# Kernel tuning notes

Hardware: AMD Instinct MI355X
Metric: run time of the kernel (lower is better)

The kernel has to match this reference:

```python
import jax, jax.numpy as jnp
import numpy as np

DIM = 1024
HEADS = 16
HEAD_DIM = DIM // HEADS


def setup_inputs() -> dict:
    key = jax.random.key(0)
    ks = jax.random.split(key, 9)
    s = 1.0 / np.sqrt(DIM)
    return {
        "x": jax.random.normal(ks[0], (2, 2048, DIM), dtype=jnp.float32),
        "Wq": jax.random.normal(ks[1], (DIM, DIM), dtype=jnp.float32) * s,
        "bq": jnp.zeros((DIM,), dtype=jnp.float32),
        "Wk": jax.random.normal(ks[2], (DIM, DIM), dtype=jnp.float32) * s,
        "bk": jnp.zeros((DIM,), dtype=jnp.float32),
        "Wv": jax.random.normal(ks[3], (DIM, DIM), dtype=jnp.float32) * s,
        "bv": jnp.zeros((DIM,), dtype=jnp.float32),
        "Wo": jax.random.normal(ks[4], (DIM, DIM), dtype=jnp.float32) * s,
        "bo": jnp.zeros((DIM,), dtype=jnp.float32),
    }


def reference(x, Wq, bq, Wk, bk, Wv, bv, Wo, bo):
    B, S, D = x.shape
    H, Dh = HEADS, HEAD_DIM

    def split_heads(t):  # (B,S,D) -> (B,H,S,Dh)
        return t.reshape(B, S, H, Dh).transpose(0, 2, 1, 3)

    q = split_heads(x @ Wq + bq)
    k = split_heads(x @ Wk + bk)
    v = split_heads(x @ Wv + bv)

    scores = jnp.einsum("bhsd,bhtd->bhst", q, k) / np.sqrt(Dh).astype(x.dtype)
    attn = jax.nn.softmax(scores, axis=-1)
    ctx = jnp.einsum("bhst,bhtd->bhsd", attn, v)
    ctx = ctx.transpose(0, 2, 1, 3).reshape(B, S, D)
    return ctx @ Wo + bo
```

## Files before the change

### kernel.cpp

```cpp
#include <hip/hip_runtime.h>
#include <hip/hip_bf16.h>
#include <cstdint>

typedef __bf16 bf16;
typedef __bf16 bf16x8 __attribute__((ext_vector_type(8)));
typedef float f32x4 __attribute__((ext_vector_type(4)));
typedef float f32x8 __attribute__((ext_vector_type(8)));
typedef float f32x16 __attribute__((ext_vector_type(16)));

#define DIM   1024
#define SEQ   2048
#define BATCH 2
#define HEADS 16
#define HDIM  64

#define QSCALE 0.1803368801111204f

__device__ __forceinline__ void gload_lds16(const void* g, void* l) {
    __builtin_amdgcn_global_load_lds(
        (const __attribute__((address_space(1))) void*)g,
        (__attribute__((address_space(3))) void*)l,
        16, 0, 0);
}

__device__ __forceinline__ uint32_t pkbf(float a, float b) {
    union { bf16 h[2]; uint32_t u; } t;
    t.h[0] = (bf16)a; t.h[1] = (bf16)b;
    return t.u;
}

#define LO8(v)  __builtin_shufflevector(v, v, 0, 1, 2, 3, 4, 5, 6, 7)
#define HI8(v)  __builtin_shufflevector(v, v, 8, 9, 10, 11, 12, 13, 14, 15)
#define LO4(v)  __builtin_shufflevector(v, v, 0, 1, 2, 3)
#define HI4(v)  __builtin_shufflevector(v, v, 4, 5, 6, 7)

__global__ __launch_bounds__(256) void cvt_wt_kernel(const float* __restrict__ Wq,
                                                     const float* __restrict__ Wk,
                                                     const float* __restrict__ Wv,
                                                     const float* __restrict__ Wo,
                                                     bf16* __restrict__ Wt) {
    int z = blockIdx.z;
    const float* W = (z == 0) ? Wq : (z == 1) ? Wk : (z == 2) ? Wv : Wo;
    bf16* out = Wt + (size_t)z * DIM * DIM;
    int w = threadIdx.x >> 6, lane = threadIdx.x & 63;
    int n  = blockIdx.x * 64 + lane;
    int kb = blockIdx.y * 32 + w * 8;
    bf16x8 o;
#pragma unroll
    for (int j = 0; j < 8; ++j)
        o[j] = (bf16)W[(size_t)(kb + j) * DIM + n];
    *(bf16x8*)(out + (size_t)n * DIM + kb) = o;
}

template <int MODE>
__global__ __launch_bounds__(256) void gemm128_kernel(
        const void* __restrict__ Ap,
        const bf16* __restrict__ WtB,
        const float* __restrict__ b0,
        const float* __restrict__ b1,
        const float* __restrict__ b2,
        void* __restrict__ outp) {
    constexpr int K = DIM;
    int z = (MODE == 0) ? blockIdx.z : 0;
    const bf16* Bt = WtB + (size_t)z * DIM * DIM;
    const float* bias = (MODE == 0) ? ((z == 0) ? b0 : (z == 1) ? b1 : b2) : b0;

    int m0 = blockIdx.y * 128, n0 = blockIdx.x * 128;
    int tid = threadIdx.x;
    int w = tid >> 6, lane = tid & 63, l15 = lane & 15, l4 = lane >> 4;
    int wr = (w >> 1) * 64, wc = (w & 1) * 64;

    __shared__ __align__(16) bf16 As[128 * 32];
    __shared__ __align__(16) bf16 Bs[128 * 32];

    int arow = tid >> 1, acol = (tid & 1) * 16;
    const float* asrc = (MODE == 0)
        ? (const float*)Ap + (size_t)(m0 + arow) * K + acol : nullptr;

    f32x4 acc[4][4] = {};

    for (int k0 = 0; k0 < K; k0 += 32) {
#pragma unroll
        for (int r = 0; r < 2; ++r) {
            int c = r * 256 + tid;
            gload_lds16(Bt + (size_t)(n0 + (c >> 2)) * K + k0 + (c & 3) * 8, &Bs[c * 8]);
        }
        if constexpr (MODE == 0) {
            const float4* s4 = (const float4*)(asrc + k0);
            float4 f0 = s4[0], f1 = s4[1], f2 = s4[2], f3 = s4[3];
            bf16x8 e0, e1;
            e0[0] = (bf16)f0.x; e0[1] = (bf16)f0.y; e0[2] = (bf16)f0.z; e0[3] = (bf16)f0.w;
            e0[4] = (bf16)f1.x; e0[5] = (bf16)f1.y; e0[6] = (bf16)f1.z; e0[7] = (bf16)f1.w;
            e1[0] = (bf16)f2.x; e1[1] = (bf16)f2.y; e1[2] = (bf16)f2.z; e1[3] = (bf16)f2.w;
            e1[4] = (bf16)f3.x; e1[5] = (bf16)f3.y; e1[6] = (bf16)f3.z; e1[7] = (bf16)f3.w;
            *(bf16x8*)&As[arow * 32 + acol]     = e0;
            *(bf16x8*)&As[arow * 32 + acol + 8] = e1;
        } else {
            const bf16* A = (const bf16*)Ap;
#pragma unroll
            for (int r = 0; r < 2; ++r) {
                int c = r * 256 + tid;
                gload_lds16(A + (size_t)(m0 + (c >> 2)) * K + k0 + (c & 3) * 8, &As[c * 8]);
            }
        }
        __syncthreads();
        bf16x8 af[4], bfr[4];
#pragma unroll
        for (int m = 0; m < 4; ++m)
            af[m] = *(const bf16x8*)&As[(wr + m * 16 + l15) * 32 + l4 * 8];
#pragma unroll
        for (int n = 0; n < 4; ++n)
            bfr[n] = *(const bf16x8*)&Bs[(wc + n * 16 + l15) * 32 + l4 * 8];
#pragma unroll
        for (int m = 0; m < 4; ++m)
#pragma unroll
            for (int n = 0; n < 4; ++n)
                acc[m][n] = __builtin_amdgcn_mfma_f32_16x16x32_bf16(
                    af[m], bfr[n], acc[m][n], 0, 0, 0);
        __syncthreads();
    }

    float oscale = (MODE == 0 && z == 0) ? QSCALE : 1.0f;
#pragma unroll
    for (int n = 0; n < 4; ++n) {
        int col = n0 + wc + n * 16 + l15;
        float bv = bias[col];
#pragma unroll
        for (int m = 0; m < 4; ++m) {
            int rowb = m0 + wr + m * 16 + l4 * 4;
            if (MODE == 1) {
                float* out = (float*)outp;
#pragma unroll
                for (int i = 0; i < 4; ++i)
                    out[(size_t)(rowb + i) * DIM + col] = acc[m][n][i] + bv;
            } else if (z == 0) {
                bf16* out = (bf16*)outp;
                int h = col >> 6, d = col & 63;
#pragma unroll
                for (int i = 0; i < 4; ++i) {
                    int row = rowb + i;
                    int bb = row >> 11, s = row & 2047;
                    out[(((size_t)(bb * HEADS + h)) * SEQ + s) * HDIM + d] =
                        (bf16)((acc[m][n][i] + bv) * oscale);
                }
            } else if (z == 1) {
                char* out = (char*)outp + (size_t)(BATCH * HEADS * SEQ * HDIM) * 2;
                int h = col >> 6, d = col & 63;
                int ks = d >> 4, lbase = ((d >> 3) & 1) * 32, e = d & 7;
#pragma unroll
                for (int i = 0; i < 4; ++i) {
                    int row = rowb + i;
                    int bb = row >> 11, s = row & 2047;
                    int hb2 = bb * HEADS + h;
                    size_t off = (size_t)(hb2 * 64 + (s >> 5)) * 4096
                                 + ks * 1024 + ((s & 31) + lbase) * 16 + e * 2;
                    *(bf16*)(out + off) = (bf16)(acc[m][n][i] + bv);
                }
            } else {
                char* out = (char*)outp + (size_t)2 * (BATCH * HEADS * SEQ * HDIM) * 2;
                int h = col >> 6, d = col & 63;
                int dblk = d >> 5;
                int bb = rowb >> 11, s0 = rowb & 2047;
                int hb2 = bb * HEADS + h;
                int lane2 = (d & 31) + 32 * ((s0 >> 3) & 1);
                size_t off = (size_t)(hb2 * 64 + (s0 >> 5)) * 4096
                             + (dblk * 2 + ((s0 >> 4) & 1)) * 1024
                             + lane2 * 16 + (s0 & 7) * 2;
                union { bf16 hh[4]; ushort4 v; } pk;
#pragma unroll
                for (int i = 0; i < 4; ++i) pk.hh[i] = (bf16)(acc[m][n][i] + bv);
                *(ushort4*)(out + off) = pk.v;
            }
        }
    }
}

__global__ __launch_bounds__(256, 4) void attn_kernel(const bf16* __restrict__ Q,
                                                      const bf16* __restrict__ Kf,
                                                      const bf16* __restrict__ Vf,
                                                      bf16* __restrict__ opA,
                                                      bf16* __restrict__ opB,
                                                      float* __restrict__ lbuf) {
    int bid = blockIdx.x;
    int xcd = bid & 7, i = bid >> 3;
    int hb  = xcd * 4 + (i >> 5);
    int rem = i & 31;
    int q0  = (rem >> 1) * 128;
    int si  = rem & 1;
    int bb = hb >> 4, h = hb & 15;
    int tid = threadIdx.x, w = tid >> 6, lane = tid & 63;
    int l31 = lane & 31, hi = lane >> 5;

    const bf16* Qh = Q + (size_t)hb * SEQ * HDIM;
    const char* kj = (const char*)Kf + (size_t)(hb * 64 + si * 32) * 4096 + lane * 16;
    const char* vj = (const char*)Vf + (size_t)(hb * 64 + si * 32) * 4096 + lane * 16;

    int qrow = q0 + w * 32 + l31;
    bf16x8 qf[4];
#pragma unroll
    for (int ks = 0; ks < 4; ++ks)
        qf[ks] = *(const bf16x8*)&Qh[(size_t)qrow * HDIM + ks * 16 + hi * 8];

    f32x16 o0 = {}, o1 = {};
    float l = 0.f;

    for (int j = 0; j < 32; ++j) {
        bf16x8 k0 = *(const bf16x8*)(kj);
        bf16x8 k1 = *(const bf16x8*)(kj + 1024);
        bf16x8 k2 = *(const bf16x8*)(kj + 2048);
        bf16x8 k3 = *(const bf16x8*)(kj + 3072);
        bf16x8 v0 = *(const bf16x8*)(vj);
        bf16x8 v1 = *(const bf16x8*)(vj + 1024);
        bf16x8 v2 = *(const bf16x8*)(vj + 2048);
        bf16x8 v3 = *(const bf16x8*)(vj + 3072);
        kj += 4096; vj += 4096;

        f32x16 s0 = {};
        __builtin_amdgcn_s_setprio(1);
        s0 = __builtin_amdgcn_mfma_f32_32x32x16_bf16(k0, qf[0], s0, 0, 0, 0);
        s0 = __builtin_amdgcn_mfma_f32_32x32x16_bf16(k1, qf[1], s0, 0, 0, 0);
        s0 = __builtin_amdgcn_mfma_f32_32x32x16_bf16(k2, qf[2], s0, 0, 0, 0);
        s0 = __builtin_amdgcn_mfma_f32_32x32x16_bf16(k3, qf[3], s0, 0, 0, 0);
        __builtin_amdgcn_s_setprio(0);

#pragma unroll
        for (int r = 0; r < 16; ++r)
            s0[r] = __builtin_amdgcn_exp2f(s0[r]);

        f32x8 a8 = LO8(s0) + HI8(s0);
        f32x4 a4 = LO4(a8) + HI4(a8);
        l += (a4[0] + a4[1]) + (a4[2] + a4[3]);

        bf16x8 pa0, pa1;
        {
            uint32_t w0 = pkbf(s0[0], s0[1]), w1 = pkbf(s0[2], s0[3]);
            uint32_t w2 = pkbf(s0[4], s0[5]), w3 = pkbf(s0[6], s0[7]);
            asm("v_permlane32_swap_b32 %0, %1" : "+v"(w0), "+v"(w2));
            asm("v_permlane32_swap_b32 %0, %1" : "+v"(w1), "+v"(w3));
            union { uint32_t u[4]; bf16x8 v; } t2;
            t2.u[0] = w0; t2.u[1] = w1; t2.u[2] = w2; t2.u[3] = w3;
            pa0 = t2.v;
            uint32_t u0 = pkbf(s0[8], s0[9]),   u1 = pkbf(s0[10], s0[11]);
            uint32_t u2 = pkbf(s0[12], s0[13]), u3 = pkbf(s0[14], s0[15]);
            asm("v_permlane32_swap_b32 %0, %1" : "+v"(u0), "+v"(u2));
            asm("v_permlane32_swap_b32 %0, %1" : "+v"(u1), "+v"(u3));
            union { uint32_t u[4]; bf16x8 v; } t3;
            t3.u[0] = u0; t3.u[1] = u1; t3.u[2] = u2; t3.u[3] = u3;
            pa1 = t3.v;
        }

        __builtin_amdgcn_s_setprio(1);
        o0 = __builtin_amdgcn_mfma_f32_32x32x16_bf16(v0, pa0, o0, 0, 0, 0);
        o0 = __builtin_amdgcn_mfma_f32_32x32x16_bf16(v1, pa1, o0, 0, 0, 0);
        o1 = __builtin_amdgcn_mfma_f32_32x32x16_bf16(v2, pa0, o1, 0, 0, 0);
        o1 = __builtin_amdgcn_mfma_f32_32x32x16_bf16(v3, pa1, o1, 0, 0, 0);
        __builtin_amdgcn_s_setprio(0);
    }

    l += __shfl_xor(l, 32);
    bf16* op = si ? opB : opA;
    if (hi == 0)
        lbuf[((size_t)si * BATCH * HEADS + hb) * SEQ + qrow] = l;
    size_t base = ((size_t)bb * SEQ + qrow) * DIM + h * HDIM;
#pragma unroll
    for (int g = 0; g < 4; ++g) {
        int dh0 = 8 * g + 4 * hi;
        union { bf16 hh[4]; ushort4 u; } a, b2;
#pragma unroll
        for (int i = 0; i < 4; ++i) {
            a.hh[i]  = (bf16)o0[4 * g + i];
            b2.hh[i] = (bf16)o1[4 * g + i];
        }
        *(ushort4*)&op[base + dh0]      = a.u;
        *(ushort4*)&op[base + 32 + dh0] = b2.u;
    }
}

__global__ __launch_bounds__(256) void merge_kernel(const bf16* __restrict__ opA,
                                                    const bf16* __restrict__ opB,
                                                    const float* __restrict__ lbuf,
                                                    bf16* __restrict__ ctx) {
    int idx = blockIdx.x * 256 + threadIdx.x;
    size_t e8 = (size_t)idx * 8;
    int row = (int)(e8 >> 10);
    int d   = (int)(e8 & 1023);
    int h = d >> 6;
    int bb = row >> 11, s = row & 2047;
    int hb = bb * HEADS + h;
    float la = lbuf[(size_t)hb * SEQ + s];
    float lb = lbuf[((size_t)BATCH * HEADS + hb) * SEQ + s];
    float inv = 1.0f / (la + lb);
    bf16x8 a = *(const bf16x8*)&opA[e8];
    bf16x8 b = *(const bf16x8*)&opB[e8];
    bf16x8 o;
#pragma unroll
    for (int i = 0; i < 8; ++i)
        o[i] = (bf16)(((float)a[i] + (float)b[i]) * inv);
    *(bf16x8*)&ctx[e8] = o;
}

extern "C" void kernel_launch(void* const* d_in, const int* in_sizes, int n_in,
                              void* d_out, int out_size, void* d_ws, size_t ws_size,
                              hipStream_t stream) {
    const float* x  = (const float*)d_in[0];
    const float* Wq = (const float*)d_in[1];
    const float* bq = (const float*)d_in[2];
    const float* Wk = (const float*)d_in[3];
    const float* bk = (const float*)d_in[4];
    const float* Wv = (const float*)d_in[5];
    const float* bv = (const float*)d_in[6];
    const float* Wo = (const float*)d_in[7];
    const float* bo = (const float*)d_in[8];

    char* ws = (char*)d_ws;
    bf16* Wt  = (bf16*)(ws + (8u  << 20));
    bf16* Qb  = (bf16*)(ws + (16u << 20));
    bf16* Kf  = (bf16*)(ws + (24u << 20));
    bf16* Vf  = (bf16*)(ws + (32u << 20));
    bf16* ctx = (bf16*)(ws + (40u << 20));

    bf16*  opA  = ctx;
    bf16*  opB  = (bf16*)ws;
    float* lbuf = (float*)Wt;

    cvt_wt_kernel<<<dim3(16, 32, 4), 256, 0, stream>>>(Wq, Wk, Wv, Wo, Wt);
    gemm128_kernel<0><<<dim3(8, 32, 3), 256, 0, stream>>>(x, Wt, bq, bk, bv, (void*)Qb);
    attn_kernel<<<1024, 256, 0, stream>>>(Qb, Kf, Vf, opA, opB, lbuf);
    merge_kernel<<<2048, 256, 0, stream>>>(opA, opB, lbuf, ctx);
    gemm128_kernel<1><<<dim3(8, 32, 1), 256, 0, stream>>>(
        ctx, Wt + (size_t)3 * DIM * DIM, bo, bo, bo, (void*)d_out);
}
```

Before: 129.1 us.

## Process two query tiles per wave in attention and fuse split-merge into output GEMM

Each attention wave now handles 64 query rows (two 32-row tiles) sharing the same K/V register loads. This halves the grid and the K/V fetch traffic per query row, at the cost of higher register pressure; the occupancy hint in the launch bounds is dropped. The separate merge kernel is removed. The output GEMM now loads both partial attention outputs, sums them, scales by the inverse softmax denominator and writes the bf16 result to shared memory. This avoids writing and re-reading the context buffer, but the GEMM's A-operand path changes from async global-to-LDS loads to register loads plus arithmetic.

Result: slower. 149.5 us (+15.9%).

```diff
diff --git a/kernel.cpp b/kernel.cpp
--- a/kernel.cpp
+++ b/kernel.cpp
@@ -55,6 +55,8 @@
 template <int MODE>
 __global__ __launch_bounds__(256) void gemm128_kernel(
         const void* __restrict__ Ap,
+        const void* __restrict__ A2p,
+        const float* __restrict__ lb,
         const bf16* __restrict__ WtB,
         const float* __restrict__ b0,
         const float* __restrict__ b1,
@@ -74,15 +76,16 @@
     __shared__ __align__(16) bf16 Bs[128 * 32];
 
     int arow = tid >> 1, acol = (tid & 1) * 16;
+    int r = m0 + arow;
     const float* asrc = (MODE == 0)
-        ? (const float*)Ap + (size_t)(m0 + arow) * K + acol : nullptr;
+        ? (const float*)Ap + (size_t)r * K + acol : nullptr;
 
     f32x4 acc[4][4] = {};
 
     for (int k0 = 0; k0 < K; k0 += 32) {
 #pragma unroll
-        for (int r = 0; r < 2; ++r) {
-            int c = r * 256 + tid;
+        for (int rr = 0; rr < 2; ++rr) {
+            int c = rr * 256 + tid;
             gload_lds16(Bt + (size_t)(n0 + (c >> 2)) * K + k0 + (c & 3) * 8, &Bs[c * 8]);
         }
         if constexpr (MODE == 0) {
@@ -96,12 +99,22 @@
             *(bf16x8*)&As[arow * 32 + acol]     = e0;
             *(bf16x8*)&As[arow * 32 + acol + 8] = e1;
         } else {
-            const bf16* A = (const bf16*)Ap;
-#pragma unroll
-            for (int r = 0; r < 2; ++r) {
-                int c = r * 256 + tid;
-                gload_lds16(A + (size_t)(m0 + (c >> 2)) * K + k0 + (c & 3) * 8, &As[c * 8]);
+            int s = r & (SEQ - 1), bbq = r >> 11;
+            int hb2 = bbq * HEADS + ((k0 + acol) >> 6);
+            float linv = 1.0f / (lb[(size_t)hb2 * SEQ + s]
+                               + lb[((size_t)BATCH * HEADS + hb2) * SEQ + s]);
+            const bf16* p0 = (const bf16*)Ap  + (size_t)r * DIM + k0 + acol;
+            const bf16* p1 = (const bf16*)A2p + (size_t)r * DIM + k0 + acol;
+            bf16x8 u0 = *(const bf16x8*)p0, u1 = *(const bf16x8*)(p0 + 8);
+            bf16x8 t0 = *(const bf16x8*)p1, t1 = *(const bf16x8*)(p1 + 8);
+            bf16x8 e0, e1;
+#pragma unroll
+            for (int i2 = 0; i2 < 8; ++i2) {
+                e0[i2] = (bf16)(((float)u0[i2] + (float)t0[i2]) * linv);
+                e1[i2] = (bf16)(((float)u1[i2] + (float)t1[i2]) * linv);
             }
+            *(bf16x8*)&As[arow * 32 + acol]     = e0;
+            *(bf16x8*)&As[arow * 32 + acol + 8] = e1;
         }
         __syncthreads();
         bf16x8 af[4], bfr[4];
@@ -175,17 +188,17 @@
     }
 }
 
-__global__ __launch_bounds__(256, 4) void attn_kernel(const bf16* __restrict__ Q,
-                                                      const bf16* __restrict__ Kf,
-                                                      const bf16* __restrict__ Vf,
-                                                      bf16* __restrict__ opA,
-                                                      bf16* __restrict__ opB,
-                                                      float* __restrict__ lbuf) {
+__global__ __launch_bounds__(256) void attn_kernel(const bf16* __restrict__ Q,
+                                                   const bf16* __restrict__ Kf,
+                                                   const bf16* __restrict__ Vf,
+                                                   bf16* __restrict__ op0,
+                                                   bf16* __restrict__ op1,
+                                                   float* __restrict__ lbuf) {
     int bid = blockIdx.x;
     int xcd = bid & 7, i = bid >> 3;
-    int hb  = xcd * 4 + (i >> 5);
-    int rem = i & 31;
-    int q0  = (rem >> 1) * 128;
+    int hb  = xcd * 4 + (i >> 4);
+    int rem = i & 15;
+    int q0  = (rem >> 1) * 256;
     int si  = rem & 1;
     int bb = hb >> 4, h = hb & 15;
     int tid = threadIdx.x, w = tid >> 6, lane = tid & 63;
@@ -195,108 +208,133 @@
     const char* kj = (const char*)Kf + (size_t)(hb * 64 + si * 32) * 4096 + lane * 16;
     const char* vj = (const char*)Vf + (size_t)(hb * 64 + si * 32) * 4096 + lane * 16;
 
-    int qrow = q0 + w * 32 + l31;
-    bf16x8 qf[4];
-#pragma unroll
-    for (int ks = 0; ks < 4; ++ks)
-        qf[ks] = *(const bf16x8*)&Qh[(size_t)qrow * HDIM + ks * 16 + hi * 8];
-
-    f32x16 o0 = {}, o1 = {};
-    float l = 0.f;
+    int qrowA = q0 + w * 64 + l31;
+    int qrowB = qrowA + 32;
+    bf16x8 qfA[4], qfB[4];
+#pragma unroll
+    for (int ks = 0; ks < 4; ++ks) {
+        qfA[ks] = *(const bf16x8*)&Qh[(size_t)qrowA * HDIM + ks * 16 + hi * 8];
+        qfB[ks] = *(const bf16x8*)&Qh[(size_t)qrowB * HDIM + ks * 16 + hi * 8];
+    }
+
+    f32x16 oA0 = {}, oA1 = {}, oB0 = {}, oB1 = {};
+    float lA = 0.f, lB = 0.f;
 
     for (int j = 0; j < 32; ++j) {
         bf16x8 k0 = *(const bf16x8*)(kj);
         bf16x8 k1 = *(const bf16x8*)(kj + 1024);
         bf16x8 k2 = *(const bf16x8*)(kj + 2048);
         bf16x8 k3 = *(const bf16x8*)(kj + 3072);
+        kj += 4096;
+
+        f32x16 sA = {}, sB = {};
+        __builtin_amdgcn_s_setprio(1);
+        sA = __builtin_amdgcn_mfma_f32_32x32x16_bf16(k0, qfA[0], sA, 0, 0, 0);
+        sA = __builtin_amdgcn_mfma_f32_32x32x16_bf16(k1, qfA[1], sA, 0, 0, 0);
+        sA = __builtin_amdgcn_mfma_f32_32x32x16_bf16(k2, qfA[2], sA, 0, 0, 0);
+        sA = __builtin_amdgcn_mfma_f32_32x32x16_bf16(k3, qfA[3], sA, 0, 0, 0);
+        sB = __builtin_amdgcn_mfma_f32_32x32x16_bf16(k0, qfB[0], sB, 0, 0, 0);
+        sB = __builtin_amdgcn_mfma_f32_32x32x16_bf16(k1, qfB[1], sB, 0, 0, 0);
+        sB = __builtin_amdgcn_mfma_f32_32x32x16_bf16(k2, qfB[2], sB, 0, 0, 0);
+        sB = __builtin_amdgcn_mfma_f32_32x32x16_bf16(k3, qfB[3], sB, 0, 0, 0);
+        __builtin_amdgcn_s_setprio(0);
+
         bf16x8 v0 = *(const bf16x8*)(vj);
         bf16x8 v1 = *(const bf16x8*)(vj + 1024);
         bf16x8 v2 = *(const bf16x8*)(vj + 2048);
         bf16x8 v3 = *(const bf16x8*)(vj + 3072);
-        kj += 4096; vj += 4096;
-
-        f32x16 s0 = {};
-        __builtin_amdgcn_s_setprio(1);
-        s0 = __builtin_amdgcn_mfma_f32_32x32x16_bf16(k0, qf[0], s0, 0, 0, 0);
-        s0 = __builtin_amdgcn_mfma_f32_32x32x16_bf16(k1, qf[1], s0, 0, 0, 0);
-        s0 = __builtin_amdgcn_mfma_f32_32x32x16_bf16(k2, qf[2], s0, 0, 0, 0);
-        s0 = __builtin_amdgcn_mfma_f32_32x32x16_bf16(k3, qf[3], s0, 0, 0, 0);
-        __builtin_amdgcn_s_setprio(0);
+        vj += 4096;
 
 #pragma unroll
         for (int r = 0; r < 16; ++r)
-            s0[r] = __builtin_amdgcn_exp2f(s0[r]);
-
-        f32x8 a8 = LO8(s0) + HI8(s0);
-        f32x4 a4 = LO4(a8) + HI4(a8);
-        l += (a4[0] + a4[1]) + (a4[2] + a4[3]);
-
-        bf16x8 pa0, pa1;
+            sA[r] = __builtin_amdgcn_exp2f(sA[r]);
         {
-            uint32_t w0 = pkbf(s0[0], s0[1]), w1 = pkbf(s0[2], s0[3]);
-            uint32_t w2 = pkbf(s0[4], s0[5]), w3 = pkbf(s0[6], s0[7]);
+            f32x8 a8 = LO8(sA) + HI8(sA);
+            f32x4 a4 = LO4(a8) + HI4(a8);
+            lA += (a4[0] + a4[1]) + (a4[2] + a4[3]);
+        }
+        bf16x8 paA0, paA1;
+        {
+            uint32_t w0 = pkbf(sA[0], sA[1]), w1 = pkbf(sA[2], sA[3]);
+            uint32_t w2 = pkbf(sA[4], sA[5]), w3 = pkbf(sA[6], sA[7]);
             asm("v_permlane32_swap_b32 %0, %1" : "+v"(w0), "+v"(w2));
             asm("v_permlane32_swap_b32 %0, %1" : "+v"(w1), "+v"(w3));
             union { uint32_t u[4]; bf16x8 v; } t2;
             t2.u[0] = w0; t2.u[1] = w1; t2.u[2] = w2; t2.u[3] = w3;
-            pa0 = t2.v;
-            uint32_t u0 = pkbf(s0[8], s0[9]),   u1 = pkbf(s0[10], s0[11]);
-            uint32_t u2 = pkbf(s0[12], s0[13]), u3 = pkbf(s0[14], s0[15]);
+            paA0 = t2.v;
+            uint32_t u0 = pkbf(sA[8], sA[9]),   u1 = pkbf(sA[10], sA[11]);
+            uint32_t u2 = pkbf(sA[12], sA[13]), u3 = pkbf(sA[14], sA[15]);
             asm("v_permlane32_swap_b32 %0, %1" : "+v"(u0), "+v"(u2));
             asm("v_permlane32_swap_b32 %0, %1" : "+v"(u1), "+v"(u3));
             union { uint32_t u[4]; bf16x8 v; } t3;
             t3.u[0] = u0; t3.u[1] = u1; t3.u[2] = u2; t3.u[3] = u3;
-            pa1 = t3.v;
-        }
-
+            paA1 = t3.v;
+        }
         __builtin_amdgcn_s_setprio(1);
-        o0 = __builtin_amdgcn_mfma_f32_32x32x16_bf16(v0, pa0, o0, 0, 0, 0);
-        o0 = __builtin_amdgcn_mfma_f32_32x32x16_bf16(v1, pa1, o0, 0, 0, 0);
-        o1 = __builtin_amdgcn_mfma_f32_32x32x16_bf16(v2, pa0, o1, 0, 0, 0);
-        o1 = __builtin_amdgcn_mfma_f32_32x32x16_bf16(v3, pa1, o1, 0, 0, 0);
+        oA0 = __builtin_amdgcn_mfma_f32_32x32x16_bf16(v0, paA0, oA0, 0, 0, 0);
+        oA0 = __builtin_amdgcn_mfma_f32_32x32x16_bf16(v1, paA1, oA0, 0, 0, 0);
+        oA1 = __builtin_amdgcn_mfma_f32_32x32x16_bf16(v2, paA0, oA1, 0, 0, 0);
+        oA1 = __builtin_amdgcn_mfma_f32_32x32x16_bf16(v3, paA1, oA1, 0, 0, 0);
         __builtin_amdgcn_s_setprio(0);
-    }
-
-    l += __shfl_xor(l, 32);
-    bf16* op = si ? opB : opA;
-    if (hi == 0)
-        lbuf[((size_t)si * BATCH * HEADS + hb) * SEQ + qrow] = l;
-    size_t base = ((size_t)bb * SEQ + qrow) * DIM + h * HDIM;
+
+#pragma unroll
+        for (int r = 0; r < 16; ++r)
+            sB[r] = __builtin_amdgcn_exp2f(sB[r]);
+        {
+            f32x8 a8 = LO8(sB) + HI8(sB);
+            f32x4 a4 = LO4(a8) + HI4(a8);
+            lB += (a4[0] + a4[1]) + (a4[2] + a4[3]);
+        }
+        bf16x8 paB0, paB1;
+        {
+            uint32_t w0 = pkbf(sB[0], sB[1]), w1 = pkbf(sB[2], sB[3]);
+            uint32_t w2 = pkbf(sB[4], sB[5]), w3 = pkbf(sB[6], sB[7]);
+            asm("v_permlane32_swap_b32 %0, %1" : "+v"(w0), "+v"(w2));
+            asm("v_permlane32_swap_b32 %0, %1" : "+v"(w1), "+v"(w3));
+            union { uint32_t u[4]; bf16x8 v; } t2;
+            t2.u[0] = w0; t2.u[1] = w1; t2.u[2] = w2; t2.u[3] = w3;
+            paB0 = t2.v;
+            uint32_t u0 = pkbf(sB[8], sB[9]),   u1 = pkbf(sB[10], sB[11]);
+            uint32_t u2 = pkbf(sB[12], sB[13]), u3 = pkbf(sB[14], sB[15]);
+            asm("v_permlane32_swap_b32 %0, %1" : "+v"(u0), "+v"(u2));
+            asm("v_permlane32_swap_b32 %0, %1" : "+v"(u1), "+v"(u3));
+            union { uint32_t u[4]; bf16x8 v; } t3;
+            t3.u[0] = u0; t3.u[1] = u1; t3.u[2] = u2; t3.u[3] = u3;
+            paB1 = t3.v;
+        }
+        __builtin_amdgcn_s_setprio(1);
+        oB0 = __builtin_amdgcn_mfma_f32_32x32x16_bf16(v0, paB0, oB0, 0, 0, 0);
+        oB0 = __builtin_amdgcn_mfma_f32_32x32x16_bf16(v1, paB1, oB0, 0, 0, 0);
+        oB1 = __builtin_amdgcn_mfma_f32_32x32x16_bf16(v2, paB0, oB1, 0, 0, 0);
+        oB1 = __builtin_amdgcn_mfma_f32_32x32x16_bf16(v3, paB1, oB1, 0, 0, 0);
+        __builtin_amdgcn_s_setprio(0);
+    }
+
+    lA += __shfl_xor(lA, 32);
+    lB += __shfl_xor(lB, 32);
+    bf16* op = si ? op1 : op0;
+    if (hi == 0) {
+        lbuf[((size_t)si * BATCH * HEADS + hb) * SEQ + qrowA] = lA;
+        lbuf[((size_t)si * BATCH * HEADS + hb) * SEQ + qrowB] = lB;
+    }
+    size_t baseA = ((size_t)bb * SEQ + qrowA) * DIM + h * HDIM;
+    size_t baseB = ((size_t)bb * SEQ + qrowB) * DIM + h * HDIM;
 #pragma unroll
     for (int g = 0; g < 4; ++g) {
         int dh0 = 8 * g + 4 * hi;
-        union { bf16 hh[4]; ushort4 u; } a, b2;
+        union { bf16 hh[4]; ushort4 u; } a0, a1, b0, b1;
 #pragma unroll
         for (int i = 0; i < 4; ++i) {
-            a.hh[i]  = (bf16)o0[4 * g + i];
-            b2.hh[i] = (bf16)o1[4 * g + i];
-        }
-        *(ushort4*)&op[base + dh0]      = a.u;
-        *(ushort4*)&op[base + 32 + dh0] = b2.u;
-    }
-}
-
-__global__ __launch_bounds__(256) void merge_kernel(const bf16* __restrict__ opA,
-                                                    const bf16* __restrict__ opB,
-                                                    const float* __restrict__ lbuf,
-                                                    bf16* __restrict__ ctx) {
-    int idx = blockIdx.x * 256 + threadIdx.x;
-    size_t e8 = (size_t)idx * 8;
-    int row = (int)(e8 >> 10);
-    int d   = (int)(e8 & 1023);
-    int h = d >> 6;
-    int bb = row >> 11, s = row & 2047;
-    int hb = bb * HEADS + h;
-    float la = lbuf[(size_t)hb * SEQ + s];
-    float lb = lbuf[((size_t)BATCH * HEADS + hb) * SEQ + s];
-    float inv = 1.0f / (la + lb);
-    bf16x8 a = *(const bf16x8*)&opA[e8];
-    bf16x8 b = *(const bf16x8*)&opB[e8];
-    bf16x8 o;
-#pragma unroll
-    for (int i = 0; i < 8; ++i)
-        o[i] = (bf16)(((float)a[i] + (float)b[i]) * inv);
-    *(bf16x8*)&ctx[e8] = o;
+            a0.hh[i] = (bf16)oA0[4 * g + i];
+            a1.hh[i] = (bf16)oA1[4 * g + i];
+            b0.hh[i] = (bf16)oB0[4 * g + i];
+            b1.hh[i] = (bf16)oB1[4 * g + i];
+        }
+        *(ushort4*)&op[baseA + dh0]      = a0.u;
+        *(ushort4*)&op[baseA + 32 + dh0] = a1.u;
+        *(ushort4*)&op[baseB + dh0]      = b0.u;
+        *(ushort4*)&op[baseB + 32 + dh0] = b1.u;
+    }
 }
 
 extern "C" void kernel_launch(void* const* d_in, const int* in_sizes, int n_in,
@@ -313,20 +351,18 @@
     const float* bo = (const float*)d_in[8];
 
     char* ws = (char*)d_ws;
-    bf16* Wt  = (bf16*)(ws + (8u  << 20));
-    bf16* Qb  = (bf16*)(ws + (16u << 20));
-    bf16* Kf  = (bf16*)(ws + (24u << 20));
-    bf16* Vf  = (bf16*)(ws + (32u << 20));
-    bf16* ctx = (bf16*)(ws + (40u << 20));
-
-    bf16*  opA  = ctx;
-    bf16*  opB  = (bf16*)ws;
-    float* lbuf = (float*)Wt;
+    bf16*  op0  = (bf16*)ws;
+    bf16*  Wt   = (bf16*)(ws + (8u  << 20));
+    float* lbuf = (float*)(ws + (8u  << 20));
+    bf16*  Qb   = (bf16*)(ws + (16u << 20));
+    bf16*  Kf   = (bf16*)(ws + (24u << 20));
+    bf16*  Vf   = (bf16*)(ws + (32u << 20));
+    bf16*  op1  = (bf16*)(ws + (40u << 20));
 
     cvt_wt_kernel<<<dim3(16, 32, 4), 256, 0, stream>>>(Wq, Wk, Wv, Wo, Wt);
-    gemm128_kernel<0><<<dim3(8, 32, 3), 256, 0, stream>>>(x, Wt, bq, bk, bv, (void*)Qb);
-    attn_kernel<<<1024, 256, 0, stream>>>(Qb, Kf, Vf, opA, opB, lbuf);
-    merge_kernel<<<2048, 256, 0, stream>>>(opA, opB, lbuf, ctx);
+    gemm128_kernel<0><<<dim3(8, 32, 3), 256, 0, stream>>>(
+        x, nullptr, nullptr, Wt, bq, bk, bv, (void*)Qb);
+    attn_kernel<<<512, 256, 0, stream>>>(Qb, Kf, Vf, op0, op1, lbuf);
     gemm128_kernel<1><<<dim3(8, 32, 1), 256, 0, stream>>>(
-        ctx, Wt + (size_t)3 * DIM * DIM, bo, bo, bo, (void*)d_out);
-}
+        op0, op1, lbuf, Wt + (size_t)3 * DIM * DIM, bo, bo, bo, (void*)d_out);
+}
```
